# Performance work log

Hardware: AMD Instinct MI355X
Metric: run time of the kernel (lower is better)

## Reference

```python
import jax, jax.numpy as jnp
import numpy as np

FP8 = jnp.float8_e4m3fn
M, H = 65536, 1024

def setup_inputs() -> dict:
    key = jax.random.key(0)
    k1, k2 = jax.random.split(key)
    inp = jax.random.normal(k1, (M, H), dtype=jnp.float16)
    weight = (jax.random.normal(k2, (H, H), dtype=jnp.float32) * 0.05)
    scale_b = jnp.ones((1, H), dtype=jnp.float32)
    return {"input": inp, "weight": weight, "scale_b": scale_b}

def reference(input, weight, scale_b):
    # fp8 cast of the activation (as in input.to(FP8_DTYPE))
    a_fp8 = input.astype(FP8)
    # tensor_model_parallel_all_gather(dim=0): identity for world_size=1
    gathered = a_fp8
    # weight stored in fp8 in the original module
    b_fp8 = weight.astype(FP8)
    # torch._scaled_mm: out = (scale_a * a) @ (b * scale_b), accumulated in fp32,
    # cast to out_dtype. scale_a is all-ones per-row, scale_b per-column.
    a = gathered.astype(jnp.float32)
    b = b_fp8.astype(jnp.float32)
    scale_a = jnp.ones((gathered.shape[0], 1), dtype=jnp.float32)
    out = (a @ b) * scale_a * scale_b  # [M, H] fp32 accumulate
    return out.astype(jnp.float16)
```

## Files before the change

### kernel.cpp

```cpp
#include <hip/hip_runtime.h>

typedef float __attribute__((ext_vector_type(4))) f32x4;
typedef unsigned int __attribute__((ext_vector_type(2))) u32x2;
typedef int __attribute__((ext_vector_type(4))) i32x4;
typedef int __attribute__((ext_vector_type(8))) i32x8;

#define M_DIM 65536
#define N_DIM 1024
#define K_DIM 1024

#define BM 64

#define WS_NEEDED ((size_t)K_DIM * N_DIM)
#define SCALE_ONE 0x7F7F7F7F

__device__ inline unsigned int cvt4(float f0, float f1, float f2, float f3) {
    int r = __builtin_amdgcn_cvt_pk_fp8_f32(f0, f1, 0, false);
    r = __builtin_amdgcn_cvt_pk_fp8_f32(f2, f3, r, true);
    return (unsigned int)r;
}

__global__ __launch_bounds__(256) void quant_w_kernel(const float* __restrict__ w,
                                                      unsigned char* __restrict__ out) {
    const int idx = blockIdx.x * 256 + threadIdx.x;
    const int t = idx >> 10, n = idx & 1023;
    const float* wp = w + (size_t)(t * 16) * N_DIM + n;
    unsigned int r[4];
#pragma unroll
    for (int q = 0; q < 4; ++q) {
        float f0 = wp[(size_t)(q * 4 + 0) * N_DIM];
        float f1 = wp[(size_t)(q * 4 + 1) * N_DIM];
        float f2 = wp[(size_t)(q * 4 + 2) * N_DIM];
        float f3 = wp[(size_t)(q * 4 + 3) * N_DIM];
        r[q] = cvt4(f0, f1, f2, f3);
    }
    i32x4 v; v.x = (int)r[0]; v.y = (int)r[1]; v.z = (int)r[2]; v.w = (int)r[3];
    ((i32x4*)out)[idx] = v;
}

__global__ __launch_bounds__(512) void gemm_fused2_kernel(const float* __restrict__ A,
                                                          const unsigned char* __restrict__ B8,
                                                          const float* __restrict__ scale_b,
                                                          float* __restrict__ out) {
    __shared__ __attribute__((aligned(16))) unsigned char sA[BM * K_DIM];

    const int tid = threadIdx.x;
    const int l = tid & 63;
    const int wid = tid >> 6;
    const int lr = l & 15;
    const int lg = l >> 4;
    const int wr2 = wid >> 2;
    const int wc2 = wid & 3;
    const int m0 = blockIdx.x * BM;

#pragma unroll
    for (int j = 0; j < 32; ++j) {
        const int u = tid + j * 512;
        const int row = u >> 8;
        const int kq = u & 255;
        const f32x4 v = *(const f32x4*)(A + (size_t)(m0 + row) * K_DIM + kq * 4);
        const unsigned int w = cvt4(v[0], v[1], v[2], v[3]);
        const int k = kq * 4;
        *(unsigned int*)(sA + row * 1024 + (((k >> 4) ^ (row & 7)) << 4) + (k & 15)) = w;
    }
    __syncthreads();

    for (int ch = 0; ch < 8; ++ch) {
        const int nb = ch * 128;
        f32x4 acc[2][2];
#pragma unroll
        for (int i = 0; i < 2; ++i)
#pragma unroll
            for (int j = 0; j < 2; ++j) acc[i][j] = (f32x4)0.0f;

#pragma unroll
        for (int t = 0; t < 8; ++t) {
            i32x8 af[2], bf[2];
#pragma unroll
            for (int mi = 0; mi < 2; ++mi) {
                const int row = wr2 * 32 + mi * 16 + lr;
                const i32x4 a0 = *(const i32x4*)(sA + row * 1024 +
                                                 (t * 8 + ((2 * lg + 0) ^ (row & 7))) * 16);
                const i32x4 a1 = *(const i32x4*)(sA + row * 1024 +
                                                 (t * 8 + ((2 * lg + 1) ^ (row & 7))) * 16);
                af[mi] = __builtin_shufflevector(a0, a1, 0, 1, 2, 3, 4, 5, 6, 7);
            }
#pragma unroll
            for (int nj = 0; nj < 2; ++nj) {
                const int n = nb + wc2 * 32 + nj * 16 + lr;
                const int kt16 = t * 8 + lg * 2;
                const i32x4 b0 = *(const i32x4*)(B8 + ((size_t)kt16 * N_DIM + n) * 16);
                const i32x4 b1 = *(const i32x4*)(B8 + ((size_t)(kt16 + 1) * N_DIM + n) * 16);
                bf[nj] = __builtin_shufflevector(b0, b1, 0, 1, 2, 3, 4, 5, 6, 7);
            }
#pragma unroll
            for (int mi = 0; mi < 2; ++mi)
#pragma unroll
                for (int nj = 0; nj < 2; ++nj)
                    acc[mi][nj] = __builtin_amdgcn_mfma_scale_f32_16x16x128_f8f6f4(
                        af[mi], bf[nj], acc[mi][nj], 0, 0,
                        0, SCALE_ONE, 0, SCALE_ONE);
        }

#pragma unroll
        for (int nj = 0; nj < 2; ++nj) {
            const int col = nb + wc2 * 32 + nj * 16 + lr;
            const float sc = scale_b[col];
#pragma unroll
            for (int mi = 0; mi < 2; ++mi) {
                const int row = m0 + wr2 * 32 + mi * 16 + lg * 4;
#pragma unroll
                for (int r = 0; r < 4; ++r) {
                    const float v = acc[mi][nj][r] * sc;
                    out[(size_t)(row + r) * N_DIM + col] = (float)(_Float16)v;
                }
            }
        }
    }
}

__global__ __launch_bounds__(256) void gemm_fused_kernel(const float* __restrict__ A,
                                                         const float* __restrict__ W,
                                                         const float* __restrict__ scale_b,
                                                         float* __restrict__ out) {
    __shared__ __attribute__((aligned(16))) unsigned char sA[128 * 64];
    __shared__ __attribute__((aligned(16))) unsigned char sB[64 * 128];

    const int tid = threadIdx.x;
    const int l = tid & 63;
    const int wid = tid >> 6;
    const int lr = l & 15;
    const int lg = l >> 4;
    const int wr = wid >> 1;
    const int wc = wid & 1;
    const int n0 = blockIdx.x * 128;
    const int m0 = blockIdx.y * 128;

    f32x4 acc[4][4];
#pragma unroll
    for (int i = 0; i < 4; ++i)
#pragma unroll
        for (int j = 0; j < 4; ++j) acc[i][j] = (f32x4)0.0f;

    const int a_g = tid & 7;
    const int a_rb = tid >> 3;
    const int aswz = lr & 6;

    for (int kt = 0; kt < K_DIM / 64; ++kt) {
        const int k0 = kt * 64;
#pragma unroll
        for (int o = 0; o < 4; ++o) {
            const int row = o * 32 + a_rb;
            const float* ap = A + (size_t)(m0 + row) * K_DIM + k0 + a_g * 8;
            const f32x4 v0 = *(const f32x4*)ap;
            const f32x4 v1 = *(const f32x4*)(ap + 4);
            u32x2 r;
            r.x = cvt4(v0[0], v0[1], v0[2], v0[3]);
            r.y = cvt4(v1[0], v1[1], v1[2], v1[3]);
            *(u32x2*)(sA + row * 64 + ((a_g ^ (row & 6)) * 8)) = r;
        }
#pragma unroll
        for (int o = 0; o < 4; ++o) {
            const int e = o * 256 + tid;
            const int g = e >> 7;
            const int n = e & 127;
            const float* wp = W + (size_t)(k0 + g * 8) * N_DIM + n0 + n;
            float f[8];
#pragma unroll
            for (int j = 0; j < 8; ++j) f[j] = wp[(size_t)j * N_DIM];
            u32x2 r;
            r.x = cvt4(f[0], f[1], f[2], f[3]);
            r.y = cvt4(f[4], f[5], f[6], f[7]);
            *(u32x2*)(sB + g * 1024 + n * 8) = r;
        }
        __syncthreads();

#pragma unroll
        for (int kk = 0; kk < 2; ++kk) {
            long long af[4], bfr[4];
            const int gread = kk * 4 + lg;
#pragma unroll
            for (int mi = 0; mi < 4; ++mi) {
                const int m = wr * 64 + mi * 16 + lr;
                af[mi] = *(const long long*)(sA + m * 64 + ((gread ^ aswz) * 8));
            }
#pragma unroll
            for (int nj = 0; nj < 4; ++nj) {
                const int n = wc * 64 + nj * 16 + lr;
                bfr[nj] = *(const long long*)(sB + gread * 1024 + n * 8);
            }
#pragma unroll
            for (int mi = 0; mi < 4; ++mi)
#pragma unroll
                for (int nj = 0; nj < 4; ++nj)
                    acc[mi][nj] = __builtin_amdgcn_mfma_f32_16x16x32_fp8_fp8(
                        af[mi], bfr[nj], acc[mi][nj], 0, 0, 0);
        }
        __syncthreads();
    }

#pragma unroll
    for (int nj = 0; nj < 4; ++nj) {
        const int col = n0 + wc * 64 + nj * 16 + lr;
        const float sc = scale_b[col];
#pragma unroll
        for (int mi = 0; mi < 4; ++mi) {
            const int row = m0 + wr * 64 + mi * 16 + lg * 4;
#pragma unroll
            for (int r = 0; r < 4; ++r) {
                const float v = acc[mi][nj][r] * sc;
                out[(size_t)(row + r) * N_DIM + col] = (float)(_Float16)v;
            }
        }
    }
}

extern "C" void kernel_launch(void* const* d_in, const int* in_sizes, int n_in,
                              void* d_out, int out_size, void* d_ws, size_t ws_size,
                              hipStream_t stream) {
    (void)out_size;
    const void* pA = d_in[0];
    const void* pW = (n_in > 1) ? d_in[1] : d_in[0];
    const void* pS = (n_in > 2) ? d_in[2] : d_in[0];
    for (int i = 0; i < n_in && i < 3; ++i) {
        if (in_sizes[i] == M_DIM * K_DIM) pA = d_in[i];
        else if (in_sizes[i] == K_DIM * N_DIM) pW = d_in[i];
        else if (in_sizes[i] == N_DIM) pS = d_in[i];
    }
    const float* A = (const float*)pA;
    const float* W = (const float*)pW;
    const float* sb = (const float*)pS;
    float* out = (float*)d_out;

    if (ws_size >= WS_NEEDED && d_ws != nullptr) {
        unsigned char* W8 = (unsigned char*)d_ws;
        quant_w_kernel<<<256, 256, 0, stream>>>(W, W8);
        gemm_fused2_kernel<<<M_DIM / BM, 512, 0, stream>>>(A, W8, sb, out);
    } else {
        gemm_fused_kernel<<<dim3(N_DIM / 128, M_DIM / 128), 256, 0, stream>>>(A, W, sb, out);
    }
}
```

Baseline: 178.3 us.

## Make fused GEMM persistent over four row tiles with double-buffered A prefetch

Each block now processes four 64-row tiles instead of one. It double-buffers the fp8-converted A tile in shared memory and issues the global loads for the next tile while computing the current one. Warp tiling also changes: each wave covers all 64 rows and 32 columns per 256-column chunk, so each B fragment load feeds more MFMAs. The goal is to hide the A load and convert latency and cut B reloads, at the cost of 128KB of LDS (one block per CU), more registers, and four times fewer blocks.

```diff
diff --git a/kernel.cpp b/kernel.cpp
--- a/kernel.cpp
+++ b/kernel.cpp
@@ -42,81 +42,105 @@
                                                           const unsigned char* __restrict__ B8,
                                                           const float* __restrict__ scale_b,
                                                           float* __restrict__ out) {
-    __shared__ __attribute__((aligned(16))) unsigned char sA[BM * K_DIM];
+    __shared__ __attribute__((aligned(16))) unsigned char sA[2][BM * K_DIM];
 
     const int tid = threadIdx.x;
     const int l = tid & 63;
     const int wid = tid >> 6;
     const int lr = l & 15;
     const int lg = l >> 4;
-    const int wr2 = wid >> 2;
-    const int wc2 = wid & 3;
-    const int m0 = blockIdx.x * BM;
-
-#pragma unroll
-    for (int j = 0; j < 32; ++j) {
-        const int u = tid + j * 512;
-        const int row = u >> 8;
-        const int kq = u & 255;
-        const f32x4 v = *(const f32x4*)(A + (size_t)(m0 + row) * K_DIM + kq * 4);
-        const unsigned int w = cvt4(v[0], v[1], v[2], v[3]);
-        const int k = kq * 4;
-        *(unsigned int*)(sA + row * 1024 + (((k >> 4) ^ (row & 7)) << 4) + (k & 15)) = w;
+
+#define STAGE_LOAD(PBASE, G, REGS)                                                      \
+    _Pragma("unroll") for (int i = 0; i < 8; ++i) {                                     \
+        const int u = tid + ((G) * 8 + i) * 512;                                        \
+        REGS[i] = *(const f32x4*)((PBASE) + (size_t)(u >> 8) * K_DIM + (u & 255) * 4);  \
+    }
+#define STAGE_WRITE(BUF, G, REGS)                                                       \
+    _Pragma("unroll") for (int i = 0; i < 8; ++i) {                                     \
+        const int u = tid + ((G) * 8 + i) * 512;                                        \
+        const int row = u >> 8;                                                         \
+        const int k = (u & 255) * 4;                                                    \
+        const unsigned int wv = cvt4(REGS[i][0], REGS[i][1], REGS[i][2], REGS[i][3]);   \
+        *(unsigned int*)(sA[BUF] + row * 1024 + (((k >> 4) ^ (row & 7)) << 4) + (k & 15)) = wv; \
+    }
+
+    {
+        const float* p0 = A + (size_t)(blockIdx.x * 4) * BM * K_DIM;
+        f32x4 rg[8];
+#pragma unroll
+        for (int g = 0; g < 4; ++g) {
+            STAGE_LOAD(p0, g, rg);
+            STAGE_WRITE(0, g, rg);
+        }
     }
     __syncthreads();
 
-    for (int ch = 0; ch < 8; ++ch) {
-        const int nb = ch * 128;
-        f32x4 acc[2][2];
-#pragma unroll
-        for (int i = 0; i < 2; ++i)
-#pragma unroll
-            for (int j = 0; j < 2; ++j) acc[i][j] = (f32x4)0.0f;
-
-#pragma unroll
-        for (int t = 0; t < 8; ++t) {
-            i32x8 af[2], bf[2];
-#pragma unroll
-            for (int mi = 0; mi < 2; ++mi) {
-                const int row = wr2 * 32 + mi * 16 + lr;
-                const i32x4 a0 = *(const i32x4*)(sA + row * 1024 +
-                                                 (t * 8 + ((2 * lg + 0) ^ (row & 7))) * 16);
-                const i32x4 a1 = *(const i32x4*)(sA + row * 1024 +
-                                                 (t * 8 + ((2 * lg + 1) ^ (row & 7))) * 16);
-                af[mi] = __builtin_shufflevector(a0, a1, 0, 1, 2, 3, 4, 5, 6, 7);
-            }
+    for (int p = 0; p < 4; ++p) {
+        const int cur = p & 1;
+        const int m0 = (blockIdx.x * 4 + p) * BM;
+        const float* pnext = A + (size_t)(m0 + BM) * K_DIM;
+        const bool more = (p < 3);
+
+#pragma unroll
+        for (int ch = 0; ch < 4; ++ch) {
+            f32x4 rg[8];
+            if (more) STAGE_LOAD(pnext, ch, rg);
+
+            const int nb = ch * 256 + wid * 32;
+            f32x4 acc[4][2];
+#pragma unroll
+            for (int i = 0; i < 4; ++i)
+#pragma unroll
+                for (int j = 0; j < 2; ++j) acc[i][j] = (f32x4)0.0f;
+
+#pragma unroll
+            for (int t = 0; t < 8; ++t) {
+                i32x8 bf[2];
+#pragma unroll
+                for (int nj = 0; nj < 2; ++nj) {
+                    const int n = nb + nj * 16 + lr;
+                    const int kt16 = t * 8 + lg * 2;
+                    const i32x4 b0 = *(const i32x4*)(B8 + ((size_t)kt16 * N_DIM + n) * 16);
+                    const i32x4 b1 = *(const i32x4*)(B8 + ((size_t)(kt16 + 1) * N_DIM + n) * 16);
+                    bf[nj] = __builtin_shufflevector(b0, b1, 0, 1, 2, 3, 4, 5, 6, 7);
+                }
+#pragma unroll
+                for (int mi = 0; mi < 4; ++mi) {
+                    const int row = mi * 16 + lr;
+                    const i32x4 a0 = *(const i32x4*)(sA[cur] + row * 1024 +
+                                                     (t * 8 + ((2 * lg + 0) ^ (row & 7))) * 16);
+                    const i32x4 a1 = *(const i32x4*)(sA[cur] + row * 1024 +
+                                                     (t * 8 + ((2 * lg + 1) ^ (row & 7))) * 16);
+                    const i32x8 af = __builtin_shufflevector(a0, a1, 0, 1, 2, 3, 4, 5, 6, 7);
+#pragma unroll
+                    for (int nj = 0; nj < 2; ++nj)
+                        acc[mi][nj] = __builtin_amdgcn_mfma_scale_f32_16x16x128_f8f6f4(
+                            af, bf[nj], acc[mi][nj], 0, 0,
+                            0, SCALE_ONE, 0, SCALE_ONE);
+                }
+            }
+
 #pragma unroll
             for (int nj = 0; nj < 2; ++nj) {
-                const int n = nb + wc2 * 32 + nj * 16 + lr;
-                const int kt16 = t * 8 + lg * 2;
-                const i32x4 b0 = *(const i32x4*)(B8 + ((size_t)kt16 * N_DIM + n) * 16);
-                const i32x4 b1 = *(const i32x4*)(B8 + ((size_t)(kt16 + 1) * N_DIM + n) * 16);
-                bf[nj] = __builtin_shufflevector(b0, b1, 0, 1, 2, 3, 4, 5, 6, 7);
-            }
-#pragma unroll
-            for (int mi = 0; mi < 2; ++mi)
-#pragma unroll
-                for (int nj = 0; nj < 2; ++nj)
-                    acc[mi][nj] = __builtin_amdgcn_mfma_scale_f32_16x16x128_f8f6f4(
-                        af[mi], bf[nj], acc[mi][nj], 0, 0,
-                        0, SCALE_ONE, 0, SCALE_ONE);
-        }
-
-#pragma unroll
-        for (int nj = 0; nj < 2; ++nj) {
-            const int col = nb + wc2 * 32 + nj * 16 + lr;
-            const float sc = scale_b[col];
-#pragma unroll
-            for (int mi = 0; mi < 2; ++mi) {
-                const int row = m0 + wr2 * 32 + mi * 16 + lg * 4;
-#pragma unroll
-                for (int r = 0; r < 4; ++r) {
-                    const float v = acc[mi][nj][r] * sc;
-                    out[(size_t)(row + r) * N_DIM + col] = (float)(_Float16)v;
+                const int col = nb + nj * 16 + lr;
+                const float sc = scale_b[col];
+#pragma unroll
+                for (int mi = 0; mi < 4; ++mi) {
+                    const int row = m0 + mi * 16 + lg * 4;
+#pragma unroll
+                    for (int r = 0; r < 4; ++r) {
+                        const float v = acc[mi][nj][r] * sc;
+                        out[(size_t)(row + r) * N_DIM + col] = (float)(_Float16)v;
+                    }
                 }
             }
-        }
-    }
+
+            if (more) STAGE_WRITE(cur ^ 1, ch, rg);
+        }
+        __syncthreads();
+    }
+#undef STAGE_LOAD
+#undef STAGE_WRITE
 }
 
 __global__ __launch_bounds__(256) void gemm_fused_kernel(const float* __restrict__ A,
@@ -235,7 +259,7 @@
     if (ws_size >= WS_NEEDED && d_ws != nullptr) {
         unsigned char* W8 = (unsigned char*)d_ws;
         quant_w_kernel<<<256, 256, 0, stream>>>(W, W8);
-        gemm_fused2_kernel<<<M_DIM / BM, 512, 0, stream>>>(A, W8, sb, out);
+        gemm_fused2_kernel<<<M_DIM / (BM * 4), 512, 0, stream>>>(A, W8, sb, out);
     } else {
         gemm_fused_kernel<<<dim3(N_DIM / 128, M_DIM / 128), 256, 0, stream>>>(A, W, sb, out);
     }
```

Result: slower. 457.8 us (+156.7%).
